# Kernel tuning notes

Hardware: AMD Instinct MI355X
Metric: run time of the kernel (lower is better)

## Reference

```python
import jax, jax.numpy as jnp
import numpy as np

NUM_HEADS = 8
EPS = 1e-5


def setup_inputs() -> dict:
    key = jax.random.key(0)
    ks = jax.random.split(key, 6)
    B, C, H, W = 8, 256, 32, 32
    s = 1.0 / np.sqrt(C)  # fan-in scale for 1x1 conv weights
    return {
        "x": jax.random.normal(ks[0], (B, C, H, W), jnp.float32),
        "Wq": jax.random.normal(ks[1], (C, C), jnp.float32) * s,
        "bq": jnp.zeros((C,), jnp.float32),
        "Wk": jax.random.normal(ks[2], (C, C), jnp.float32) * s,
        "bk": jnp.zeros((C,), jnp.float32),
        "Wv": jax.random.normal(ks[3], (C, C), jnp.float32) * s,
        "bv": jnp.zeros((C,), jnp.float32),
        "Wp": jax.random.normal(ks[4], (C, C), jnp.float32) * s,
        "bp": jnp.zeros((C,), jnp.float32),
        "gamma": jnp.ones((C,), jnp.float32),
        "beta": jnp.zeros((C,), jnp.float32),
    }


def _conv1x1(x, W, b):
    # 1x1 Conv2d == channel-mixing matmul: [B,C,H,W] -> [B,C,H,W]
    return jnp.einsum('oi,bihw->bohw', W, x) + b[None, :, None, None]


def reference(x, Wq, bq, Wk, bk, Wv, bv, Wp, bp, gamma, beta):
    B, C, H, W = x.shape
    nh = NUM_HEADS
    hd = C // nh
    HW = H * W

    q = _conv1x1(x, Wq, bq).reshape(B, nh, hd, HW)
    k = _conv1x1(x, Wk, bk).reshape(B, nh, hd, HW)
    v = _conv1x1(x, Wv, bv).reshape(B, nh, hd, HW)

    scores = jnp.einsum('bhdi,bhdj->bhij', q, k) / (hd ** 0.5)  # [B,nh,HW,HW]
    attn = jax.nn.softmax(scores, axis=-1)
    out = jnp.einsum('bhij,bhdj->bhdi', attn, v).reshape(B, C, H, W)

    out = _conv1x1(out, Wp, bp) + x  # residual

    # LayerNorm over channel dim (channels-last, as in original)
    o = out.transpose(0, 2, 3, 1)  # [B,H,W,C]
    mu = jnp.mean(o, axis=-1, keepdims=True)
    var = jnp.var(o, axis=-1, keepdims=True)
    o = (o - mu) * jax.lax.rsqrt(var + EPS) * gamma + beta
    return o.transpose(0, 3, 1, 2)
```

## Files before the change

### kernel.cpp

```cpp
#include <hip/hip_runtime.h>
#include <math.h>

#define NB 8
#define NC 256
#define NHW 1024
#define NHEADS 8
#define HD 32

typedef _Float16 half_t;
typedef __attribute__((ext_vector_type(8))) _Float16 half8;
typedef __attribute__((ext_vector_type(4))) _Float16 half4v;
typedef __attribute__((ext_vector_type(2))) _Float16 half2v;
typedef __attribute__((ext_vector_type(4))) float floatx4;

__device__ __forceinline__ half2v pk2(float a, float b) {
    union {
        __fp16 __attribute__((ext_vector_type(2))) r;
        half2v h;
    } u;
    u.r = __builtin_amdgcn_cvt_pkrtz(a, b);
    return u.h;
}
__device__ __forceinline__ void st8h(half_t* p, half2v a, half2v b) {
    union { half2v h[2]; uint2 u; } t;
    t.h[0] = a; t.h[1] = b;
    *(uint2*)p = t.u;
}

__global__ __launch_bounds__(256) void wprep(
    const float* __restrict__ Wq, const float* __restrict__ Wk,
    const float* __restrict__ Wv, const float* __restrict__ Wp,
    half_t* __restrict__ Wh)
{
    int t = blockIdx.x * 256 + threadIdx.x;
    int e = t * 8;
    int m = e >> 16, off = e & 65535;
    const float* src = (m == 0) ? Wq : (m == 1) ? Wk : (m == 2) ? Wv : Wp;
    float sc = (m == 0) ? 0.17677669529663687f * 1.4426950408889634f : 1.f;
    float4 a = *(const float4*)(src + off);
    float4 b = *(const float4*)(src + off + 4);
    union { half2v h2[4]; half8 h8; } u;
    u.h2[0] = pk2(a.x * sc, a.y * sc);
    u.h2[1] = pk2(a.z * sc, a.w * sc);
    u.h2[2] = pk2(b.x * sc, b.y * sc);
    u.h2[3] = pk2(b.z * sc, b.w * sc);
    *(half8*)&Wh[e] = u.h8;
}

__global__ __launch_bounds__(512) void qkv_mfma(
    const float* __restrict__ x, const half_t* __restrict__ Wh,
    const float* __restrict__ bq, const float* __restrict__ bk, const float* __restrict__ bv,
    half_t* __restrict__ Qt, half_t* __restrict__ Kt, half_t* __restrict__ Vv)
{
    __shared__ half_t xs[64][264];

    int bz = blockIdx.z;
    int b = bz & 7, p = bz >> 3;
    const half_t* Wf    = Wh + (size_t)p * 65536;
    const float*  bias  = (p == 0) ? bq : (p == 1) ? bk : bv;

    int t = threadIdx.x;
    int s0 = blockIdx.x * 64;
    const float* xb = x + (size_t)b * NC * NHW;

    int wv = t >> 6, lane = t & 63;
    int mm = lane & 15, q = lane >> 4;
    int o0 = wv * 32;

    half8 af[8][2];
    #pragma unroll
    for (int kk = 0; kk < 8; kk++)
        #pragma unroll
        for (int mt = 0; mt < 2; mt++)
            af[kk][mt] = *(const half8*)&Wf[(size_t)(o0 + mt * 16 + mm) * NC + kk * 32 + q * 8];

    {
        int sf = t & 15, cp = t >> 4;
        int sw = (sf & 7) << 3;
        #pragma unroll
        for (int pass = 0; pass < 4; pass++) {
            int c = cp * 2 + 64 * pass;
            int cw = c ^ sw;
            float4 a  = *(const float4*)&xb[(size_t)c * NHW + s0 + sf * 4];
            float4 bb = *(const float4*)&xb[(size_t)(c + 1) * NHW + s0 + sf * 4];
            *(half2v*)&xs[sf * 4 + 0][cw] = pk2(a.x, bb.x);
            *(half2v*)&xs[sf * 4 + 1][cw] = pk2(a.y, bb.y);
            *(half2v*)&xs[sf * 4 + 2][cw] = pk2(a.z, bb.z);
            *(half2v*)&xs[sf * 4 + 3][cw] = pk2(a.w, bb.w);
        }
    }
    __syncthreads();

    floatx4 acc[2][4];
    #pragma unroll
    for (int mt = 0; mt < 2; mt++)
        #pragma unroll
        for (int nt = 0; nt < 4; nt++) acc[mt][nt] = (floatx4){0.f, 0.f, 0.f, 0.f};

    #pragma unroll
    for (int kk = 0; kk < 8; kk++) {
        int k0 = kk * 32;
        half8 bf[4];
        #pragma unroll
        for (int nt = 0; nt < 4; nt++) {
            int row = nt * 16 + mm;
            int col = (k0 + q * 8) ^ (((row >> 2) & 7) << 3);
            bf[nt] = *(const half8*)&xs[row][col];
        }
        #pragma unroll
        for (int mt = 0; mt < 2; mt++)
            #pragma unroll
            for (int nt = 0; nt < 4; nt++)
                acc[mt][nt] = __builtin_amdgcn_mfma_f32_16x16x32_f16(af[kk][mt], bf[nt], acc[mt][nt], 0, 0, 0);
    }

    int h  = wv;
    int bh = b * NHEADS + h;
    const float qs = 0.17677669529663687f * 1.4426950408889634f;
    float bsc = (p == 0) ? qs : 1.f;

    #pragma unroll
    for (int mt = 0; mt < 2; mt++) {
        int d0 = mt * 16 + q * 4;
        float bb[4];
        #pragma unroll
        for (int r = 0; r < 4; r++) bb[r] = bias[o0 + mt * 16 + q * 4 + r] * bsc;
        #pragma unroll
        for (int nt = 0; nt < 4; nt++) {
            int s = s0 + nt * 16 + mm;
            float v0 = acc[mt][nt][0] + bb[0], v1 = acc[mt][nt][1] + bb[1];
            float v2 = acc[mt][nt][2] + bb[2], v3 = acc[mt][nt][3] + bb[3];
            if (p < 2) {
                half_t* out = (p == 0 ? Qt : Kt) + ((size_t)bh * NHW + s) * HD + d0;
                st8h(out, pk2(v0, v1), pk2(v2, v3));
            } else {
                Vv[((size_t)bh * HD + d0 + 0) * NHW + s] = (half_t)v0;
                Vv[((size_t)bh * HD + d0 + 1) * NHW + s] = (half_t)v1;
                Vv[((size_t)bh * HD + d0 + 2) * NHW + s] = (half_t)v2;
                Vv[((size_t)bh * HD + d0 + 3) * NHW + s] = (half_t)v3;
            }
        }
    }
}

__global__ __launch_bounds__(256) void attn_mfma(
    const half_t* __restrict__ Qt, const half_t* __restrict__ Kt,
    const half_t* __restrict__ Vv, half_t* __restrict__ At)
{
    __shared__ half_t Pl[4][4][2][16][36];
    __shared__ float Oz[4][32][66];
    __shared__ float Dz[4][64];

    int wv = threadIdx.x >> 6, lane = threadIdx.x & 63;
    int mm = lane & 15, q = lane >> 4;
    int L = blockIdx.x;
    int bh = L & 63, iblk = L >> 6;
    int b = bh >> 3, h = bh & 7;
    int i0 = iblk * 64;

    const half_t* Qb = Qt + (size_t)bh * NHW * HD;
    const half_t* Kb = Kt + (size_t)bh * NHW * HD;
    const half_t* Vb = Vv + (size_t)bh * HD * NHW;

    half8 qf[4];
    #pragma unroll
    for (int qt = 0; qt < 4; qt++)
        qf[qt] = *(const half8*)&Qb[(size_t)(i0 + qt * 16 + mm) * HD + q * 8];

    const int jb = wv * 256;
    floatx4 zero = (floatx4){0.f, 0.f, 0.f, 0.f};
    floatx4 oa[4][2];
    #pragma unroll
    for (int qt = 0; qt < 4; qt++) { oa[qt][0] = zero; oa[qt][1] = zero; }
    float dd[4] = {0.f, 0.f, 0.f, 0.f};
    const _Float16 z = (_Float16)0.f;
    half8 pf[4];
    #pragma unroll
    for (int qt = 0; qt < 4; qt++) pf[qt] = (half8){z, z, z, z, z, z, z, z};

    half8 kc0 = *(const half8*)&Kb[(size_t)(jb + mm) * HD + q * 8];
    half8 kc1 = *(const half8*)&Kb[(size_t)(jb + 16 + mm) * HD + q * 8];
    half8 kn0 = *(const half8*)&Kb[(size_t)(jb + 32 + mm) * HD + q * 8];
    half8 kn1 = *(const half8*)&Kb[(size_t)(jb + 48 + mm) * HD + q * 8];
    half8 vc0 = *(const half8*)&Vb[(size_t)mm * NHW + jb + q * 8];
    half8 vc1 = *(const half8*)&Vb[(size_t)(16 + mm) * NHW + jb + q * 8];
    half8 vp0 = vc0, vp1 = vc1;

    #pragma unroll
    for (int it = 0; it < 8; it++) {
        floatx4 s[4][2];
        #pragma unroll
        for (int qt = 0; qt < 4; qt++) {
            s[qt][0] = __builtin_amdgcn_mfma_f32_16x16x32_f16(kc0, qf[qt], zero, 0, 0, 0);
            s[qt][1] = __builtin_amdgcn_mfma_f32_16x16x32_f16(kc1, qf[qt], zero, 0, 0, 0);
        }

        int jk = jb + ((it + 2) & 7) * 32;
        int jv = jb + ((it + 1) & 7) * 32;
        half8 kf0 = *(const half8*)&Kb[(size_t)(jk + mm) * HD + q * 8];
        half8 kf1 = *(const half8*)&Kb[(size_t)(jk + 16 + mm) * HD + q * 8];
        half8 vn0 = *(const half8*)&Vb[(size_t)mm * NHW + jv + q * 8];
        half8 vn1 = *(const half8*)&Vb[(size_t)(16 + mm) * NHW + jv + q * 8];

        #pragma unroll
        for (int qt = 0; qt < 4; qt++) {
            oa[qt][0] = __builtin_amdgcn_mfma_f32_16x16x32_f16(vp0, pf[qt], oa[qt][0], 0, 0, 0);
            oa[qt][1] = __builtin_amdgcn_mfma_f32_16x16x32_f16(vp1, pf[qt], oa[qt][1], 0, 0, 0);
        }

        int buf = it & 1;
        #pragma unroll
        for (int qt = 0; qt < 4; qt++) {
            float e0 = exp2f(s[qt][0][0]), e1 = exp2f(s[qt][0][1]);
            float e2 = exp2f(s[qt][0][2]), e3 = exp2f(s[qt][0][3]);
            float f0 = exp2f(s[qt][1][0]), f1 = exp2f(s[qt][1][1]);
            float f2 = exp2f(s[qt][1][2]), f3 = exp2f(s[qt][1][3]);
            dd[qt] += ((e0 + e1) + (e2 + e3)) + ((f0 + f1) + (f2 + f3));
            half_t (*PB)[36] = Pl[wv][qt][buf];
            st8h(&PB[mm][q * 4],      pk2(e0, e1), pk2(e2, e3));
            st8h(&PB[mm][16 + q * 4], pk2(f0, f1), pk2(f2, f3));
        }
        #pragma unroll
        for (int qt = 0; qt < 4; qt++) {
            union { half4v h4[2]; half8 h8; } u;
            u.h4[0] = *(half4v*)&Pl[wv][qt][buf][mm][q * 8];
            u.h4[1] = *(half4v*)&Pl[wv][qt][buf][mm][q * 8 + 4];
            pf[qt] = u.h8;
        }

        kc0 = kn0; kc1 = kn1; kn0 = kf0; kn1 = kf1;
        vp0 = vc0; vp1 = vc1; vc0 = vn0; vc1 = vn1;
    }
    #pragma unroll
    for (int qt = 0; qt < 4; qt++) {
        oa[qt][0] = __builtin_amdgcn_mfma_f32_16x16x32_f16(vp0, pf[qt], oa[qt][0], 0, 0, 0);
        oa[qt][1] = __builtin_amdgcn_mfma_f32_16x16x32_f16(vp1, pf[qt], oa[qt][1], 0, 0, 0);
    }

    #pragma unroll
    for (int qt = 0; qt < 4; qt++) {
        dd[qt] += __shfl_xor(dd[qt], 16);
        dd[qt] += __shfl_xor(dd[qt], 32);
    }

    #pragma unroll
    for (int qt = 0; qt < 4; qt++)
        #pragma unroll
        for (int r = 0; r < 4; r++) {
            Oz[wv][q * 4 + r][qt * 16 + mm]      = oa[qt][0][r];
            Oz[wv][16 + q * 4 + r][qt * 16 + mm] = oa[qt][1][r];
        }
    if (q == 0) {
        #pragma unroll
        for (int qt = 0; qt < 4; qt++) Dz[wv][qt * 16 + mm] = dd[qt];
    }
    __syncthreads();

    int t = threadIdx.x;
    int iloc = t >> 2, dg = t & 3;
    float den = (Dz[0][iloc] + Dz[1][iloc]) + (Dz[2][iloc] + Dz[3][iloc]);
    float rinv = 1.f / den;
    float v[8];
    #pragma unroll
    for (int r = 0; r < 8; r++) {
        int d = dg * 8 + r;
        v[r] = ((Oz[0][d][iloc] + Oz[1][d][iloc]) + (Oz[2][d][iloc] + Oz[3][d][iloc])) * rinv;
    }
    half_t* dst = At + ((size_t)b * NHW + i0 + iloc) * NC + h * HD + dg * 8;
    st8h(dst,     pk2(v[0], v[1]), pk2(v[2], v[3]));
    st8h(dst + 4, pk2(v[4], v[5]), pk2(v[6], v[7]));
}

__global__ __launch_bounds__(512) void projln(
    const half_t* __restrict__ At, const half_t* __restrict__ Wph,
    const float* __restrict__ bp, const float* __restrict__ x,
    const float* __restrict__ gamma, const float* __restrict__ beta,
    float* __restrict__ outp)
{
    __shared__ float tile[32][273];
    __shared__ float xs[256][33];
    __shared__ float Pz[4][64][33];
    __shared__ float ps[16][32], ps2[16][32];
    __shared__ float mu_s[32], rs_s[32];

    int t = threadIdx.x, wv = t >> 6, lane = t & 63;
    int mm = lane & 15, q = lane >> 4;
    int oh = wv & 3, kh = wv >> 2;
    int o0 = oh * 64;
    int b = blockIdx.y, s0 = blockIdx.x * 32;
    const half_t* ab = At + (size_t)b * NHW * NC;
    int kbase = kh * 128;

    half8 wf[4][4];
    #pragma unroll
    for (int kk = 0; kk < 4; kk++)
        #pragma unroll
        for (int mt = 0; mt < 4; mt++)
            wf[kk][mt] = *(const half8*)&Wph[(size_t)(o0 + mt * 16 + mm) * NC + kbase + kk * 32 + q * 8];
    half8 bf[4][2];
    #pragma unroll
    for (int kk = 0; kk < 4; kk++)
        #pragma unroll
        for (int nt = 0; nt < 2; nt++)
            bf[kk][nt] = *(const half8*)&ab[(size_t)(s0 + nt * 16 + mm) * NC + kbase + kk * 32 + q * 8];

    {
        int sL = t & 31, cb = t >> 5;
        #pragma unroll
        for (int pass = 0; pass < 16; pass++) {
            int c = pass * 16 + cb;
            xs[c][sL] = x[((size_t)b * NC + c) * NHW + s0 + sL];
        }
    }

    floatx4 acc[4][2];
    #pragma unroll
    for (int mt = 0; mt < 4; mt++)
        #pragma unroll
        for (int nt = 0; nt < 2; nt++) acc[mt][nt] = (floatx4){0.f, 0.f, 0.f, 0.f};

    #pragma unroll
    for (int kk = 0; kk < 4; kk++)
        #pragma unroll
        for (int mt = 0; mt < 4; mt++)
            #pragma unroll
            for (int nt = 0; nt < 2; nt++)
                acc[mt][nt] = __builtin_amdgcn_mfma_f32_16x16x32_f16(wf[kk][mt], bf[kk][nt], acc[mt][nt], 0, 0, 0);

    if (kh == 1) {
        #pragma unroll
        for (int mt = 0; mt < 4; mt++)
            #pragma unroll
            for (int nt = 0; nt < 2; nt++)
                #pragma unroll
                for (int r = 0; r < 4; r++)
                    Pz[oh][mt * 16 + q * 4 + r][nt * 16 + mm] = acc[mt][nt][r];
    }
    __syncthreads();
    if (kh == 0) {
        #pragma unroll
        for (int mt = 0; mt < 4; mt++) {
            #pragma unroll
            for (int nt = 0; nt < 2; nt++) {
                #pragma unroll
                for (int r = 0; r < 4; r++) {
                    int ol = mt * 16 + q * 4 + r;
                    int o = o0 + ol;
                    int sl = nt * 16 + mm;
                    tile[sl][o] = acc[mt][nt][r] + Pz[oh][ol][sl] + bp[o] + xs[o][sl];
                }
            }
        }
    }
    __syncthreads();

    int sL = t & 31, part = t >> 5;
    float sum = 0.f, sq = 0.f;
    #pragma unroll
    for (int cc = 0; cc < 16; cc++) {
        float v = tile[sL][part * 16 + cc];
        sum += v; sq += v * v;
    }
    ps[part][sL] = sum; ps2[part][sL] = sq;
    __syncthreads();
    if (t < 32) {
        float S = 0.f, S2 = 0.f;
        #pragma unroll
        for (int p2 = 0; p2 < 16; p2++) { S += ps[p2][t]; S2 += ps2[p2][t]; }
        float mu  = S * (1.f / NC);
        float var = S2 * (1.f / NC) - mu * mu;
        mu_s[t] = mu;
        rs_s[t] = rsqrtf(var + 1e-5f);
    }
    __syncthreads();
    float mu = mu_s[sL], rs = rs_s[sL];
    float* ob = outp + (size_t)b * NC * NHW;
    #pragma unroll
    for (int cc = 0; cc < 16; cc++) {
        int c = part * 16 + cc;
        ob[(size_t)c * NHW + s0 + sL] = (tile[sL][c] - mu) * rs * gamma[c] + beta[c];
    }
}

extern "C" void kernel_launch(void* const* d_in, const int* in_sizes, int n_in,
                              void* d_out, int out_size, void* d_ws, size_t ws_size,
                              hipStream_t stream)
{
    const float* x     = (const float*)d_in[0];
    const float* Wq    = (const float*)d_in[1];
    const float* bq    = (const float*)d_in[2];
    const float* Wk    = (const float*)d_in[3];
    const float* bk    = (const float*)d_in[4];
    const float* Wv    = (const float*)d_in[5];
    const float* bv    = (const float*)d_in[6];
    const float* Wp    = (const float*)d_in[7];
    const float* bp    = (const float*)d_in[8];
    const float* gamma = (const float*)d_in[9];
    const float* beta  = (const float*)d_in[10];
    float* out = (float*)d_out;

    char* w = (char*)d_ws;
    half_t* Qt = (half_t*)(w);
    half_t* Kt = (half_t*)(w + ((size_t)4  << 20));
    half_t* Vv = (half_t*)(w + ((size_t)8  << 20));
    half_t* At = (half_t*)(w + ((size_t)12 << 20));
    half_t* Wh = (half_t*)(w + ((size_t)16 << 20));

    wprep<<<dim3(128), 256, 0, stream>>>(Wq, Wk, Wv, Wp, Wh);
    qkv_mfma<<<dim3(16, 1, 24), 512, 0, stream>>>(x, Wh, bq, bk, bv, Qt, Kt, Vv);
    attn_mfma<<<dim3(1024), 256, 0, stream>>>(Qt, Kt, Vv, At);
    projln<<<dim3(32, 8), 512, 0, stream>>>(At, Wh + 3 * 65536, bp, x, gamma, beta, out);
}
```

Baseline: 128.1 us.

## Compute softmax denominators via MFMA with ones and restructure projection split

```diff
diff --git a/kernel.cpp b/kernel.cpp
--- a/kernel.cpp
+++ b/kernel.cpp
@@ -169,11 +169,12 @@
 
     const int jb = wv * 256;
     floatx4 zero = (floatx4){0.f, 0.f, 0.f, 0.f};
-    floatx4 oa[4][2];
-    #pragma unroll
-    for (int qt = 0; qt < 4; qt++) { oa[qt][0] = zero; oa[qt][1] = zero; }
-    float dd[4] = {0.f, 0.f, 0.f, 0.f};
+    floatx4 oa[4][2], dacc[4];
+    #pragma unroll
+    for (int qt = 0; qt < 4; qt++) { oa[qt][0] = zero; oa[qt][1] = zero; dacc[qt] = zero; }
     const _Float16 z = (_Float16)0.f;
+    const _Float16 o1 = (_Float16)1.f;
+    const half8 ones = {o1, o1, o1, o1, o1, o1, o1, o1};
     half8 pf[4];
     #pragma unroll
     for (int qt = 0; qt < 4; qt++) pf[qt] = (half8){z, z, z, z, z, z, z, z};
@@ -206,6 +207,7 @@
         for (int qt = 0; qt < 4; qt++) {
             oa[qt][0] = __builtin_amdgcn_mfma_f32_16x16x32_f16(vp0, pf[qt], oa[qt][0], 0, 0, 0);
             oa[qt][1] = __builtin_amdgcn_mfma_f32_16x16x32_f16(vp1, pf[qt], oa[qt][1], 0, 0, 0);
+            dacc[qt]  = __builtin_amdgcn_mfma_f32_16x16x32_f16(ones, pf[qt], dacc[qt], 0, 0, 0);
         }
 
         int buf = it & 1;
@@ -215,7 +217,6 @@
             float e2 = exp2f(s[qt][0][2]), e3 = exp2f(s[qt][0][3]);
             float f0 = exp2f(s[qt][1][0]), f1 = exp2f(s[qt][1][1]);
             float f2 = exp2f(s[qt][1][2]), f3 = exp2f(s[qt][1][3]);
-            dd[qt] += ((e0 + e1) + (e2 + e3)) + ((f0 + f1) + (f2 + f3));
             half_t (*PB)[36] = Pl[wv][qt][buf];
             st8h(&PB[mm][q * 4],      pk2(e0, e1), pk2(e2, e3));
             st8h(&PB[mm][16 + q * 4], pk2(f0, f1), pk2(f2, f3));
@@ -235,12 +236,7 @@
     for (int qt = 0; qt < 4; qt++) {
         oa[qt][0] = __builtin_amdgcn_mfma_f32_16x16x32_f16(vp0, pf[qt], oa[qt][0], 0, 0, 0);
         oa[qt][1] = __builtin_amdgcn_mfma_f32_16x16x32_f16(vp1, pf[qt], oa[qt][1], 0, 0, 0);
-    }
-
-    #pragma unroll
-    for (int qt = 0; qt < 4; qt++) {
-        dd[qt] += __shfl_xor(dd[qt], 16);
-        dd[qt] += __shfl_xor(dd[qt], 32);
+        dacc[qt]  = __builtin_amdgcn_mfma_f32_16x16x32_f16(ones, pf[qt], dacc[qt], 0, 0, 0);
     }
 
     #pragma unroll
@@ -252,7 +248,7 @@
         }
     if (q == 0) {
         #pragma unroll
-        for (int qt = 0; qt < 4; qt++) Dz[wv][qt * 16 + mm] = dd[qt];
+        for (int qt = 0; qt < 4; qt++) Dz[wv][qt * 16 + mm] = dacc[qt][0];
     }
     __syncthreads();
 
@@ -279,30 +275,14 @@
 {
     __shared__ float tile[32][273];
     __shared__ float xs[256][33];
-    __shared__ float Pz[4][64][33];
     __shared__ float ps[16][32], ps2[16][32];
     __shared__ float mu_s[32], rs_s[32];
 
     int t = threadIdx.x, wv = t >> 6, lane = t & 63;
     int mm = lane & 15, q = lane >> 4;
-    int oh = wv & 3, kh = wv >> 2;
-    int o0 = oh * 64;
+    int o0 = wv * 32;
     int b = blockIdx.y, s0 = blockIdx.x * 32;
     const half_t* ab = At + (size_t)b * NHW * NC;
-    int kbase = kh * 128;
-
-    half8 wf[4][4];
-    #pragma unroll
-    for (int kk = 0; kk < 4; kk++)
-        #pragma unroll
-        for (int mt = 0; mt < 4; mt++)
-            wf[kk][mt] = *(const half8*)&Wph[(size_t)(o0 + mt * 16 + mm) * NC + kbase + kk * 32 + q * 8];
-    half8 bf[4][2];
-    #pragma unroll
-    for (int kk = 0; kk < 4; kk++)
-        #pragma unroll
-        for (int nt = 0; nt < 2; nt++)
-            bf[kk][nt] = *(const half8*)&ab[(size_t)(s0 + nt * 16 + mm) * NC + kbase + kk * 32 + q * 8];
 
     {
         int sL = t & 31, cb = t >> 5;
@@ -313,42 +293,35 @@
         }
     }
 
-    floatx4 acc[4][2];
-    #pragma unroll
-    for (int mt = 0; mt < 4; mt++)
+    floatx4 acc[2][2];
+    #pragma unroll
+    for (int mt = 0; mt < 2; mt++)
         #pragma unroll
         for (int nt = 0; nt < 2; nt++) acc[mt][nt] = (floatx4){0.f, 0.f, 0.f, 0.f};
 
     #pragma unroll
-    for (int kk = 0; kk < 4; kk++)
-        #pragma unroll
-        for (int mt = 0; mt < 4; mt++)
+    for (int kk = 0; kk < 8; kk++) {
+        int k0 = kk * 32;
+        half8 bf0 = *(const half8*)&ab[(size_t)(s0 + mm) * NC + k0 + q * 8];
+        half8 bf1 = *(const half8*)&ab[(size_t)(s0 + 16 + mm) * NC + k0 + q * 8];
+        half8 af0 = *(const half8*)&Wph[(size_t)(o0 + mm) * NC + k0 + q * 8];
+        half8 af1 = *(const half8*)&Wph[(size_t)(o0 + 16 + mm) * NC + k0 + q * 8];
+        acc[0][0] = __builtin_amdgcn_mfma_f32_16x16x32_f16(af0, bf0, acc[0][0], 0, 0, 0);
+        acc[0][1] = __builtin_amdgcn_mfma_f32_16x16x32_f16(af0, bf1, acc[0][1], 0, 0, 0);
+        acc[1][0] = __builtin_amdgcn_mfma_f32_16x16x32_f16(af1, bf0, acc[1][0], 0, 0, 0);
+        acc[1][1] = __builtin_amdgcn_mfma_f32_16x16x32_f16(af1, bf1, acc[1][1], 0, 0, 0);
+    }
+
+    __syncthreads();
+    #pragma unroll
+    for (int mt = 0; mt < 2; mt++) {
+        #pragma unroll
+        for (int nt = 0; nt < 2; nt++) {
             #pragma unroll
-            for (int nt = 0; nt < 2; nt++)
-                acc[mt][nt] = __builtin_amdgcn_mfma_f32_16x16x32_f16(wf[kk][mt], bf[kk][nt], acc[mt][nt], 0, 0, 0);
-
-    if (kh == 1) {
-        #pragma unroll
-        for (int mt = 0; mt < 4; mt++)
-            #pragma unroll
-            for (int nt = 0; nt < 2; nt++)
-                #pragma unroll
-                for (int r = 0; r < 4; r++)
-                    Pz[oh][mt * 16 + q * 4 + r][nt * 16 + mm] = acc[mt][nt][r];
-    }
-    __syncthreads();
-    if (kh == 0) {
-        #pragma unroll
-        for (int mt = 0; mt < 4; mt++) {
-            #pragma unroll
-            for (int nt = 0; nt < 2; nt++) {
-                #pragma unroll
-                for (int r = 0; r < 4; r++) {
-                    int ol = mt * 16 + q * 4 + r;
-                    int o = o0 + ol;
-                    int sl = nt * 16 + mm;
-                    tile[sl][o] = acc[mt][nt][r] + Pz[oh][ol][sl] + bp[o] + xs[o][sl];
-                }
+            for (int r = 0; r < 4; r++) {
+                int o = o0 + mt * 16 + q * 4 + r;
+                int sl = nt * 16 + mm;
+                tile[sl][o] = acc[mt][nt][r] + bp[o] + xs[o][sl];
             }
         }
     }
```

New measurement: 128.3 us. No clear change (+0.2%).
